# Performance work log

Hardware: AMD Instinct MI355X
Metric: run time of the kernel (lower is better)

## Reference

```python
import jax, jax.numpy as jnp
import numpy as np
import math

T = 4096        # block_size / sequence length
E = 2048        # embedding_dim
D = 256         # head_dim


def setup_inputs() -> dict:
    key = jax.random.key(0)
    k_x, k_q, k_k, k_v = jax.random.split(key, 4)
    x = jax.random.normal(k_x, (T, E), dtype=jnp.float32)
    # nn.Linear weights are [out_features, in_features]
    s = 1.0 / math.sqrt(E)
    Wq = jax.random.normal(k_q, (D, E), dtype=jnp.float32) * s
    Wk = jax.random.normal(k_k, (D, E), dtype=jnp.float32) * s
    Wv = jax.random.normal(k_v, (D, E), dtype=jnp.float32) * s
    return {"x": x, "Wq": Wq, "Wk": Wk, "Wv": Wv}


def reference(x, Wq, Wk, Wv):
    # Projections: x @ W.T  (torch Linear, no bias)
    Q = x @ Wq.T            # [T, D]
    K = x @ Wk.T            # [T, D]
    V = x @ Wv.T            # [T, D]
    scale = 1.0 / math.sqrt(Q.shape[-1])
    scores = (Q @ K.T) * scale                      # [T, T]
    causal = jnp.tril(jnp.ones((T, T), dtype=bool))
    scores = jnp.where(causal, scores, jnp.float32(-1e10))
    probs = jax.nn.softmax(scores, axis=-1)         # row softmax (torch legacy dim=1 for 2-D)
    return probs @ V                                # [T, D]
```

## Files before the change

kernel.cpp:

```cpp
#include <hip/hip_runtime.h>
#include <hip/hip_bf16.h>

#define T_DIM 4096
#define E_DIM 2048
#define D_DIM 256
#define NT_SPLIT 5

typedef __attribute__((ext_vector_type(4))) float f32x4;
typedef __attribute__((ext_vector_type(8))) short s16x8;

__device__ __forceinline__ unsigned short f2bf(float f) {
  unsigned int u = __float_as_uint(f);
  unsigned int r = (u + 0x7FFFu + ((u >> 16) & 1u)) >> 16;
  return (unsigned short)r;
}
__device__ __forceinline__ float bf2f(unsigned short h) {
  return __uint_as_float(((unsigned int)h) << 16);
}

__device__ __forceinline__ f32x4 mfma16(s16x8 a, s16x8 b, f32x4 c) {
  return __builtin_amdgcn_mfma_f32_16x16x32_bf16(a, b, c, 0, 0, 0);
}

__device__ __forceinline__ void gload_lds16(const void* g, void* l) {
  __builtin_amdgcn_global_load_lds((const __attribute__((address_space(1))) void*)g,
                                   (__attribute__((address_space(3))) void*)l, 16, 0, 0);
}

__global__ __launch_bounds__(256) void cvt_all(const float* __restrict__ x,
                                               const float* __restrict__ wq,
                                               const float* __restrict__ wk,
                                               const float* __restrict__ wv,
                                               unsigned short* __restrict__ xb,
                                               unsigned short* __restrict__ wb) {
  int blk = blockIdx.x;
  const float* src;
  unsigned short* dst;
  int rel;
  if (blk < 4096)      { src = x;  dst = xb;           rel = blk; }
  else if (blk < 4352) { src = wq; dst = wb;           rel = blk - 4096; }
  else if (blk < 4608) { src = wk; dst = wb + 524288;  rel = blk - 4352; }
  else                 { src = wv; dst = wb + 1048576; rel = blk - 4608; }
  int i = rel * 256 + threadIdx.x;
  float4 a = ((const float4*)src)[i * 2];
  float4 b = ((const float4*)src)[i * 2 + 1];
  uint4 o;
  o.x = (unsigned int)f2bf(a.x) | ((unsigned int)f2bf(a.y) << 16);
  o.y = (unsigned int)f2bf(a.z) | ((unsigned int)f2bf(a.w) << 16);
  o.z = (unsigned int)f2bf(b.x) | ((unsigned int)f2bf(b.y) << 16);
  o.w = (unsigned int)f2bf(b.z) | ((unsigned int)f2bf(b.w) << 16);
  ((uint4*)dst)[i] = o;
}

__global__ __launch_bounds__(256, 3) void qkv_gemm(
    const unsigned short* __restrict__ xb, const unsigned short* __restrict__ wb,
    unsigned short* __restrict__ Qg, unsigned short* __restrict__ Kg,
    unsigned short* __restrict__ Vt) {
  __shared__ __align__(16) unsigned short Al[2][128 * 64];
  __shared__ __align__(16) unsigned short Bl[2][64 * 64];
  int tid = threadIdx.x, wid = tid >> 6, lane = tid & 63;
  int lr = lane & 15, lk = lane >> 4;
  int bi_ = (int)blockIdx.x;
  int xcd = bi_ & 7, kk = bi_ >> 3;
  int mb_ = (kk / 12) * 8 + xcd, nb_ = kk % 12;
  int bm0 = mb_ * 128, bn0 = nb_ * 64;
  int wm = (wid >> 1) * 64, wn = (wid & 1) * 32;

  f32x4 acc[4][2];
#pragma unroll
  for (int m = 0; m < 4; ++m)
#pragma unroll
    for (int n = 0; n < 2; ++n) acc[m][n] = (f32x4){0.f, 0.f, 0.f, 0.f};

#define STAGE_QKV(kt, buf)                                                              \
  {                                                                                     \
    int k0 = (kt)*64;                                                                   \
    _Pragma("unroll") for (int i2 = 0; i2 < 4; ++i2) {                                  \
      int ci = (wid * 4 + i2) * 64 + lane;                                              \
      int row = ci >> 3, cc = ci & 7;                                                   \
      gload_lds16(&xb[(size_t)(bm0 + row) * E_DIM + k0 + ((cc ^ (row & 7)) << 3)],      \
                  &Al[buf][(size_t)(wid * 4 + i2) * 512]);                              \
    }                                                                                   \
    _Pragma("unroll") for (int i2 = 0; i2 < 2; ++i2) {                                  \
      int ci = (wid * 2 + i2) * 64 + lane;                                              \
      int row = ci >> 3, cc = ci & 7;                                                   \
      gload_lds16(&wb[(size_t)(bn0 + row) * E_DIM + k0 + ((cc ^ (row & 7)) << 3)],      \
                  &Bl[buf][(size_t)(wid * 2 + i2) * 512]);                              \
    }                                                                                   \
  }

  STAGE_QKV(0, 0);
  for (int kt = 0; kt < 32; ++kt) {
    int cur = kt & 1;
    __syncthreads();
    if (kt + 1 < 32) STAGE_QKV(kt + 1, cur ^ 1);
    s16x8 af[2][4], bfr[2][2];
#pragma unroll
    for (int c = 0; c < 2; ++c) {
#pragma unroll
      for (int m = 0; m < 4; ++m)
        af[c][m] = *(const s16x8*)&Al[cur][(size_t)(wm + m * 16 + lr) * 64 +
                                           (((c * 4 + lk) ^ (lr & 7)) << 3)];
#pragma unroll
      for (int n = 0; n < 2; ++n)
        bfr[c][n] = *(const s16x8*)&Bl[cur][(size_t)(wn + n * 16 + lr) * 64 +
                                            (((c * 4 + lk) ^ (lr & 7)) << 3)];
    }
#pragma unroll
    for (int c = 0; c < 2; ++c)
#pragma unroll
      for (int m = 0; m < 4; ++m)
#pragma unroll
        for (int n = 0; n < 2; ++n) acc[m][n] = mfma16(af[c][m], bfr[c][n], acc[m][n]);
  }

#pragma unroll
  for (int m = 0; m < 4; ++m) {
    int grow = bm0 + wm + m * 16 + lk * 4;
#pragma unroll
    for (int n = 0; n < 2; ++n) {
      int gcol = bn0 + wn + n * 16 + lr;
      unsigned short h[4];
#pragma unroll
      for (int r = 0; r < 4; ++r) h[r] = f2bf(acc[m][n][r]);
      if (gcol < 256) {
#pragma unroll
        for (int r = 0; r < 4; ++r) Qg[(size_t)(grow + r) * D_DIM + gcol] = h[r];
      } else if (gcol < 512) {
#pragma unroll
        for (int r = 0; r < 4; ++r) Kg[(size_t)(grow + r) * D_DIM + gcol - 256] = h[r];
      } else {
        uint2 w;
        w.x = (unsigned int)h[0] | ((unsigned int)h[1] << 16);
        w.y = (unsigned int)h[2] | ((unsigned int)h[3] << 16);
        *(uint2*)&Vt[(size_t)(gcol - 512) * T_DIM + grow] = w;
      }
    }
  }
#undef STAGE_QKV
}

__global__ __launch_bounds__(256, 2) void attn_kernel(
    const unsigned short* __restrict__ Qg, const unsigned short* __restrict__ Kg,
    const unsigned short* __restrict__ Vt, unsigned short* __restrict__ Opart,
    float* __restrict__ mpart, float* __restrict__ lpart) {
  __shared__ __align__(16) unsigned short Kl[2][32 * 256];
  __shared__ __align__(16) unsigned short Vl[2][256 * 32];
  __shared__ __align__(16) unsigned short Pl[4][32 * 40];

  int b = blockIdx.x;
  int t = 31, s = 0;
  {
    int acc = 0;
#pragma unroll 1
    for (int k = 1; k <= 32; ++k) {
      int c = (4 * k + 4) / 5;
      if (acc + c > b) { t = k - 1; s = b - acc; break; }
      acc += c;
    }
  }
  int nt = 4 * (t + 1) - NT_SPLIT * s;
  if (nt > NT_SPLIT) nt = NT_SPLIT;

  int tid = threadIdx.x, wid = tid >> 6, lane = tid & 63;
  int lr = lane & 15, lk = lane >> 4;
  int q0w = t * 128 + wid * 32;
  unsigned short* pl = &Pl[wid][0];

  s16x8 qf[2][8];
#pragma unroll
  for (int qb = 0; qb < 2; ++qb)
#pragma unroll
    for (int c = 0; c < 8; ++c)
      qf[qb][c] = *(const s16x8*)&Qg[(size_t)(q0w + qb * 16 + lr) * D_DIM + c * 32 + lk * 8];

  float m_run[2] = {-1e30f, -1e30f}, l_run[2] = {0.f, 0.f};
  f32x4 Oa[2][16];
#pragma unroll
  for (int qb = 0; qb < 2; ++qb)
#pragma unroll
    for (int d = 0; d < 16; ++d) Oa[qb][d] = (f32x4){0.f, 0.f, 0.f, 0.f};
  const float scale = 0.0625f;
  int j0 = NT_SPLIT * s;

#define STAGE_KV(j, buf)                                                             \
  {                                                                                  \
    int kv_ = (j)*32;                                                                \
    _Pragma("unroll") for (int i2 = 0; i2 < 4; ++i2) {                               \
      int l = (wid * 4 + i2) * 64 + lane;                                            \
      int row = l >> 5, gcs = l & 31;                                                \
      gload_lds16(&Kg[(size_t)(kv_ + row) * D_DIM + ((gcs ^ (row & 7)) << 3)],       \
                  &Kl[buf][(size_t)(wid * 4 + i2) * 512]);                           \
    }                                                                                \
    _Pragma("unroll") for (int i2 = 0; i2 < 4; ++i2) {                               \
      int l = (wid * 4 + i2) * 64 + lane;                                            \
      int d_ = l >> 2, gs = l & 3;                                                   \
      gload_lds16(&Vt[(size_t)d_ * T_DIM + kv_ + ((gs ^ ((d_ >> 1) & 3)) << 3)],     \
                  &Vl[buf][(size_t)(wid * 4 + i2) * 512]);                           \
    }                                                                                \
  }

  STAGE_KV(j0, 0);
  for (int n = 0; n < nt; ++n) {
    int j = j0 + n, kv = j * 32, cur = n & 1;
    __syncthreads();
    if (n + 1 < nt) STAGE_KV(j + 1, cur ^ 1);
    const unsigned short* kl = &Kl[cur][0];
    const unsigned short* vl = &Vl[cur][0];

    f32x4 sa[2][2];
#pragma unroll
    for (int qb = 0; qb < 2; ++qb)
#pragma unroll
      for (int jb = 0; jb < 2; ++jb) sa[qb][jb] = (f32x4){0.f, 0.f, 0.f, 0.f};
    int sw = lr & 7;
#pragma unroll
    for (int jb = 0; jb < 2; ++jb) {
      int rowbase = (jb * 16 + lr) * 32;
#pragma unroll
      for (int c = 0; c < 8; ++c) {
        s16x8 kf = *(const s16x8*)&kl[(size_t)(rowbase + ((c * 4 + lk) ^ sw)) * 8];
        sa[0][jb] = mfma16(kf, qf[0][c], sa[0][jb]);
        sa[1][jb] = mfma16(kf, qf[1][c], sa[1][jb]);
      }
    }

    bool needmask = (kv + 31 > q0w);
    float alpha_s[2];
#pragma unroll
    for (int qb = 0; qb < 2; ++qb) {
      int myq = q0w + qb * 16 + lr;
      float tmax = -1e30f;
#pragma unroll
      for (int jb = 0; jb < 2; ++jb) {
#pragma unroll
        for (int r = 0; r < 4; ++r) {
          float v = sa[qb][jb][r] * scale;
          if (needmask && (kv + jb * 16 + lk * 4 + r) > myq) v = -1e30f;
          sa[qb][jb][r] = v;
          tmax = fmaxf(tmax, v);
        }
      }
      tmax = fmaxf(tmax, __shfl_xor(tmax, 16));
      tmax = fmaxf(tmax, __shfl_xor(tmax, 32));
      float m_new = fmaxf(fmaxf(m_run[qb], tmax), -1e29f);
      alpha_s[qb] = __expf(m_run[qb] - m_new);
      float psum = 0.f;
#pragma unroll
      for (int jb = 0; jb < 2; ++jb) {
        float p0 = __expf(sa[qb][jb][0] - m_new);
        float p1 = __expf(sa[qb][jb][1] - m_new);
        float p2 = __expf(sa[qb][jb][2] - m_new);
        float p3 = __expf(sa[qb][jb][3] - m_new);
        psum += (p0 + p1) + (p2 + p3);
        uint2 w;
        w.x = (unsigned int)f2bf(p0) | ((unsigned int)f2bf(p1) << 16);
        w.y = (unsigned int)f2bf(p2) | ((unsigned int)f2bf(p3) << 16);
        *(uint2*)&pl[(qb * 16 + lr) * 40 + jb * 16 + lk * 4] = w;
      }
      psum += __shfl_xor(psum, 16);
      psum += __shfl_xor(psum, 32);
      l_run[qb] = l_run[qb] * alpha_s[qb] + psum;
      m_run[qb] = m_new;
    }

    float al[2][4];
#pragma unroll
    for (int qb = 0; qb < 2; ++qb)
#pragma unroll
      for (int r = 0; r < 4; ++r) al[qb][r] = __shfl(alpha_s[qb], lk * 4 + r);
#pragma unroll
    for (int qb = 0; qb < 2; ++qb)
#pragma unroll
      for (int d = 0; d < 16; ++d) {
#pragma unroll
        for (int r = 0; r < 4; ++r) Oa[qb][d][r] *= al[qb][r];
      }

    s16x8 pf0 = *(const s16x8*)&pl[lr * 40 + lk * 8];
    s16x8 pf1 = *(const s16x8*)&pl[(16 + lr) * 40 + lk * 8];
    int vsw = lk ^ ((lr >> 1) & 3);
#pragma unroll
    for (int d = 0; d < 16; ++d) {
      s16x8 vf = *(const s16x8*)&vl[(size_t)((d * 16 + lr) * 4 + vsw) * 8];
      Oa[0][d] = mfma16(pf0, vf, Oa[0][d]);
      Oa[1][d] = mfma16(pf1, vf, Oa[1][d]);
    }
  }

#pragma unroll
  for (int d = 0; d < 16; ++d) {
#pragma unroll
    for (int qb = 0; qb < 2; ++qb) {
      unsigned short h[4];
#pragma unroll
      for (int r = 0; r < 4; ++r) h[r] = f2bf(Oa[qb][d][r]);
      uint2 w;
      w.x = (unsigned int)h[0] | ((unsigned int)h[1] << 16);
      w.y = (unsigned int)h[2] | ((unsigned int)h[3] << 16);
      *(uint2*)&Opart[((size_t)b * 256 + d * 16 + lr) * 128 + wid * 32 + qb * 16 + lk * 4] = w;
    }
  }
  if (lk == 0) {
#pragma unroll
    for (int qb = 0; qb < 2; ++qb) {
      mpart[(size_t)b * 128 + wid * 32 + qb * 16 + lr] = m_run[qb];
      lpart[(size_t)b * 128 + wid * 32 + qb * 16 + lr] = l_run[qb];
    }
  }
#undef STAGE_KV
}

__global__ __launch_bounds__(256) void merge_kernel(const unsigned short* __restrict__ Opart,
                                                    const float* __restrict__ mpart,
                                                    const float* __restrict__ lpart,
                                                    float* __restrict__ out) {
  __shared__ float trans[128 * 65];
  int blk = blockIdx.x;
  int t = blk >> 2, d0 = (blk & 3) * 64, q0 = t * 128;
  int ql = threadIdx.x & 127, dg = threadIdx.x >> 7;
  int base = 0;
#pragma unroll 1
  for (int k = 1; k <= t; ++k) base += (4 * k + 4) / 5;
  int nb = (4 * (t + 1) + 4) / 5;

  float M = -1e30f, den = 0.f;
  for (int p = 0; p < nb; ++p) {
    float mp = mpart[(size_t)(base + p) * 128 + ql];
    float lp = lpart[(size_t)(base + p) * 128 + ql];
    float Mn = fmaxf(M, mp);
    den = den * __expf(M - Mn) + __expf(mp - Mn) * lp;
    M = Mn;
  }
  float inv = 1.0f / den;

  float acc[32];
#pragma unroll
  for (int k = 0; k < 32; ++k) acc[k] = 0.f;
  for (int p = 0; p < nb; ++p) {
    float w = __expf(mpart[(size_t)(base + p) * 128 + ql] - M);
    const unsigned short* op = &Opart[((size_t)(base + p) * 256 + d0 + dg) * 128 + ql];
#pragma unroll
    for (int k = 0; k < 32; ++k) acc[k] += w * bf2f(op[(size_t)(2 * k) * 128]);
  }
#pragma unroll
  for (int k = 0; k < 32; ++k) trans[ql * 65 + dg + 2 * k] = acc[k] * inv;
  __syncthreads();

#pragma unroll
  for (int kk = 0; kk < 32; ++kk) {
    int q = (threadIdx.x >> 6) + 4 * kk;
    int dd = threadIdx.x & 63;
    out[(size_t)(q0 + q) * 256 + d0 + dd] = trans[q * 65 + dd];
  }
}

extern "C" void kernel_launch(void* const* d_in, const int* in_sizes, int n_in,
                              void* d_out, int out_size, void* d_ws, size_t ws_size,
                              hipStream_t stream) {
  const float* x  = (const float*)d_in[0];
  const float* Wq = (const float*)d_in[1];
  const float* Wk = (const float*)d_in[2];
  const float* Wv = (const float*)d_in[3];

  char* ws = (char*)d_ws;
  unsigned short* xb = (unsigned short*)(ws);
  unsigned short* wb = (unsigned short*)(ws + 16777216);
  unsigned short* Qg = (unsigned short*)(ws + 19922944);
  unsigned short* Kg = (unsigned short*)(ws + 22020096);
  unsigned short* Vt = (unsigned short*)(ws + 24117248);
  unsigned short* Opart = (unsigned short*)(ws + 26214400);
  float* mpart = (float*)(ws + 54722560);
  float* lpart = (float*)(ws + 54945280);

  cvt_all<<<4864, 256, 0, stream>>>(x, Wq, Wk, Wv, xb, wb);
  qkv_gemm<<<384, 256, 0, stream>>>(xb, wb, Qg, Kg, Vt);
  attn_kernel<<<435, 256, 0, stream>>>(Qg, Kg, Vt, Opart, mpart, lpart);
  merge_kernel<<<128, 256, 0, stream>>>(Opart, mpart, lpart, (float*)d_out);
}
```

Before: 112.6 us.

## Retile QKV GEMM and attention split, fuse merge passes into one online loop

The QKV GEMM switches to 64x64 tiles with a K-step of 128, giving 768 blocks. Its pipeline now uses explicit barriers and vmcnt waits instead of __syncthreads. Attention moves to 512-thread blocks over 256-query tiles, with 64-wide KV chunks and a fixed two-chunk split per block (272 blocks). Query-tile and split indices are mapped through a sqrt-based triangular index, and the P buffer gets an XOR-swizzled layout. The merge kernel folds its max/denominator pass and its accumulation pass into one online-rescaled loop over more partials. Together these change occupancy and per-block work balance and raise partial-output traffic, with some risk from the larger LDS footprint and register pressure.

Result: faster. 109.9 us (-2.4%).

```diff
diff --git a/kernel.cpp b/kernel.cpp
--- a/kernel.cpp
+++ b/kernel.cpp
@@ -4,7 +4,6 @@
 #define T_DIM 4096
 #define E_DIM 2048
 #define D_DIM 256
-#define NT_SPLIT 5
 
 typedef __attribute__((ext_vector_type(4))) float f32x4;
 typedef __attribute__((ext_vector_type(8))) short s16x8;
@@ -52,70 +51,72 @@
   ((uint4*)dst)[i] = o;
 }
 
-__global__ __launch_bounds__(256, 3) void qkv_gemm(
+__global__ __launch_bounds__(256, 2) void qkv_gemm(
     const unsigned short* __restrict__ xb, const unsigned short* __restrict__ wb,
     unsigned short* __restrict__ Qg, unsigned short* __restrict__ Kg,
     unsigned short* __restrict__ Vt) {
-  __shared__ __align__(16) unsigned short Al[2][128 * 64];
-  __shared__ __align__(16) unsigned short Bl[2][64 * 64];
+  __shared__ __align__(16) unsigned short Al[2][64 * 128];
+  __shared__ __align__(16) unsigned short Bl[2][64 * 128];
   int tid = threadIdx.x, wid = tid >> 6, lane = tid & 63;
   int lr = lane & 15, lk = lane >> 4;
-  int bi_ = (int)blockIdx.x;
-  int xcd = bi_ & 7, kk = bi_ >> 3;
-  int mb_ = (kk / 12) * 8 + xcd, nb_ = kk % 12;
-  int bm0 = mb_ * 128, bn0 = nb_ * 64;
-  int wm = (wid >> 1) * 64, wn = (wid & 1) * 32;
-
-  f32x4 acc[4][2];
-#pragma unroll
-  for (int m = 0; m < 4; ++m)
+  int bi = (int)blockIdx.x;
+  int j = (bi & 7) * 96 + (bi >> 3);
+  int mb = j / 12, nb = j % 12;
+  int bm0 = mb * 64, bn0 = nb * 64;
+  int wm = (wid >> 1) * 32, wn = (wid & 1) * 32;
+
+  f32x4 acc[2][2];
+#pragma unroll
+  for (int m = 0; m < 2; ++m)
 #pragma unroll
     for (int n = 0; n < 2; ++n) acc[m][n] = (f32x4){0.f, 0.f, 0.f, 0.f};
 
 #define STAGE_QKV(kt, buf)                                                              \
   {                                                                                     \
-    int k0 = (kt)*64;                                                                   \
+    int k0 = (kt)*128;                                                                  \
     _Pragma("unroll") for (int i2 = 0; i2 < 4; ++i2) {                                  \
-      int ci = (wid * 4 + i2) * 64 + lane;                                              \
-      int row = ci >> 3, cc = ci & 7;                                                   \
-      gload_lds16(&xb[(size_t)(bm0 + row) * E_DIM + k0 + ((cc ^ (row & 7)) << 3)],      \
+      int idx = (wid * 4 + i2) * 64 + lane;                                             \
+      int row = idx >> 4, g = idx & 15;                                                 \
+      gload_lds16(&xb[(size_t)(bm0 + row) * E_DIM + k0 + ((g ^ (row & 7)) << 3)],      \
                   &Al[buf][(size_t)(wid * 4 + i2) * 512]);                              \
+      gload_lds16(&wb[(size_t)(bn0 + row) * E_DIM + k0 + ((g ^ (row & 7)) << 3)],      \
+                  &Bl[buf][(size_t)(wid * 4 + i2) * 512]);                              \
     }                                                                                   \
-    _Pragma("unroll") for (int i2 = 0; i2 < 2; ++i2) {                                  \
-      int ci = (wid * 2 + i2) * 64 + lane;                                              \
-      int row = ci >> 3, cc = ci & 7;                                                   \
-      gload_lds16(&wb[(size_t)(bn0 + row) * E_DIM + k0 + ((cc ^ (row & 7)) << 3)],      \
-                  &Bl[buf][(size_t)(wid * 2 + i2) * 512]);                              \
-    }                                                                                   \
   }
 
   STAGE_QKV(0, 0);
-  for (int kt = 0; kt < 32; ++kt) {
+  for (int kt = 0; kt < 16; ++kt) {
     int cur = kt & 1;
-    __syncthreads();
-    if (kt + 1 < 32) STAGE_QKV(kt + 1, cur ^ 1);
-    s16x8 af[2][4], bfr[2][2];
-#pragma unroll
-    for (int c = 0; c < 2; ++c) {
-#pragma unroll
-      for (int m = 0; m < 4; ++m)
-        af[c][m] = *(const s16x8*)&Al[cur][(size_t)(wm + m * 16 + lr) * 64 +
+    __builtin_amdgcn_s_barrier();
+    if (kt + 1 < 16) {
+      STAGE_QKV(kt + 1, cur ^ 1);
+      asm volatile("s_waitcnt vmcnt(8)" ::: "memory");
+    } else {
+      asm volatile("s_waitcnt vmcnt(0)" ::: "memory");
+    }
+    __builtin_amdgcn_s_barrier();
+    s16x8 af[4][2], bfr[4][2];
+#pragma unroll
+    for (int c = 0; c < 4; ++c) {
+#pragma unroll
+      for (int m = 0; m < 2; ++m)
+        af[c][m] = *(const s16x8*)&Al[cur][(size_t)(wm + m * 16 + lr) * 128 +
                                            (((c * 4 + lk) ^ (lr & 7)) << 3)];
 #pragma unroll
       for (int n = 0; n < 2; ++n)
-        bfr[c][n] = *(const s16x8*)&Bl[cur][(size_t)(wn + n * 16 + lr) * 64 +
+        bfr[c][n] = *(const s16x8*)&Bl[cur][(size_t)(wn + n * 16 + lr) * 128 +
                                             (((c * 4 + lk) ^ (lr & 7)) << 3)];
     }
 #pragma unroll
-    for (int c = 0; c < 2; ++c)
-#pragma unroll
-      for (int m = 0; m < 4; ++m)
+    for (int c = 0; c < 4; ++c)
+#pragma unroll
+      for (int m = 0; m < 2; ++m)
 #pragma unroll
         for (int n = 0; n < 2; ++n) acc[m][n] = mfma16(af[c][m], bfr[c][n], acc[m][n]);
   }
 
 #pragma unroll
-  for (int m = 0; m < 4; ++m) {
+  for (int m = 0; m < 2; ++m) {
     int grow = bm0 + wm + m * 16 + lk * 4;
 #pragma unroll
     for (int n = 0; n < 2; ++n) {
@@ -140,99 +141,99 @@
 #undef STAGE_QKV
 }
 
-__global__ __launch_bounds__(256, 2) void attn_kernel(
+__global__ __launch_bounds__(512, 2) void attn_kernel(
     const unsigned short* __restrict__ Qg, const unsigned short* __restrict__ Kg,
     const unsigned short* __restrict__ Vt, unsigned short* __restrict__ Opart,
     float* __restrict__ mpart, float* __restrict__ lpart) {
-  __shared__ __align__(16) unsigned short Kl[2][32 * 256];
-  __shared__ __align__(16) unsigned short Vl[2][256 * 32];
-  __shared__ __align__(16) unsigned short Pl[4][32 * 40];
-
-  int b = blockIdx.x;
-  int t = 31, s = 0;
-  {
-    int acc = 0;
-#pragma unroll 1
-    for (int k = 1; k <= 32; ++k) {
-      int c = (4 * k + 4) / 5;
-      if (acc + c > b) { t = k - 1; s = b - acc; break; }
-      acc += c;
-    }
-  }
-  int nt = 4 * (t + 1) - NT_SPLIT * s;
-  if (nt > NT_SPLIT) nt = NT_SPLIT;
+  __shared__ __align__(16) unsigned short Kl[2][64 * 256];
+  __shared__ __align__(16) unsigned short Vl[2][256 * 64];
+  __shared__ __align__(16) unsigned short Pl[8 * 32 * 64];
+
+  int bi = (int)blockIdx.x;
+  int j = (bi & 7) * 34 + (bi >> 3);
+  int t = (int)((sqrtf(4.0f * (float)j + 1.0f) - 1.0f) * 0.5f);
+  while (t > 0 && t * (t + 1) > j) --t;
+  while ((t + 1) * (t + 2) <= j) ++t;
+  int s = j - t * (t + 1);
 
   int tid = threadIdx.x, wid = tid >> 6, lane = tid & 63;
   int lr = lane & 15, lk = lane >> 4;
-  int q0w = t * 128 + wid * 32;
-  unsigned short* pl = &Pl[wid][0];
-
-  s16x8 qf[2][8];
-#pragma unroll
-  for (int qb = 0; qb < 2; ++qb)
-#pragma unroll
-    for (int c = 0; c < 8; ++c)
-      qf[qb][c] = *(const s16x8*)&Qg[(size_t)(q0w + qb * 16 + lr) * D_DIM + c * 32 + lk * 8];
-
-  float m_run[2] = {-1e30f, -1e30f}, l_run[2] = {0.f, 0.f};
-  f32x4 Oa[2][16];
-#pragma unroll
-  for (int qb = 0; qb < 2; ++qb)
-#pragma unroll
-    for (int d = 0; d < 16; ++d) Oa[qb][d] = (f32x4){0.f, 0.f, 0.f, 0.f};
-  const float scale = 0.0625f;
-  int j0 = NT_SPLIT * s;
-
-#define STAGE_KV(j, buf)                                                             \
+  int q0w = t * 256 + wid * 32;
+  unsigned short* pl = &Pl[wid * 2048];
+
+#define STAGE_KV(jt, buf)                                                            \
   {                                                                                  \
-    int kv_ = (j)*32;                                                                \
+    int kv_ = (jt)*64;                                                               \
     _Pragma("unroll") for (int i2 = 0; i2 < 4; ++i2) {                               \
-      int l = (wid * 4 + i2) * 64 + lane;                                            \
-      int row = l >> 5, gcs = l & 31;                                                \
-      gload_lds16(&Kg[(size_t)(kv_ + row) * D_DIM + ((gcs ^ (row & 7)) << 3)],       \
+      int idx = (wid * 4 + i2) * 64 + lane;                                          \
+      int row = idx >> 5, g = idx & 31;                                              \
+      gload_lds16(&Kg[(size_t)(kv_ + row) * D_DIM + ((g ^ (row & 7)) << 3)],         \
                   &Kl[buf][(size_t)(wid * 4 + i2) * 512]);                           \
     }                                                                                \
     _Pragma("unroll") for (int i2 = 0; i2 < 4; ++i2) {                               \
-      int l = (wid * 4 + i2) * 64 + lane;                                            \
-      int d_ = l >> 2, gs = l & 3;                                                   \
-      gload_lds16(&Vt[(size_t)d_ * T_DIM + kv_ + ((gs ^ ((d_ >> 1) & 3)) << 3)],     \
+      int idx = (wid * 4 + i2) * 64 + lane;                                          \
+      int d_ = idx >> 3, g = idx & 7;                                                \
+      gload_lds16(&Vt[(size_t)d_ * T_DIM + kv_ + ((g ^ (d_ & 7)) << 3)],             \
                   &Vl[buf][(size_t)(wid * 4 + i2) * 512]);                           \
     }                                                                                \
   }
 
-  STAGE_KV(j0, 0);
-  for (int n = 0; n < nt; ++n) {
-    int j = j0 + n, kv = j * 32, cur = n & 1;
-    __syncthreads();
-    if (n + 1 < nt) STAGE_KV(j + 1, cur ^ 1);
+  STAGE_KV(2 * s, 0);
+
+  s16x8 qf[2][8];
+#pragma unroll
+  for (int qb = 0; qb < 2; ++qb)
+#pragma unroll
+    for (int c = 0; c < 8; ++c)
+      qf[qb][c] = *(const s16x8*)&Qg[(size_t)(q0w + qb * 16 + lr) * D_DIM + c * 32 + lk * 8];
+
+  float m_run[2] = {-1e30f, -1e30f}, l_run[2] = {0.f, 0.f};
+  f32x4 Oa[2][16];
+#pragma unroll
+  for (int qb = 0; qb < 2; ++qb)
+#pragma unroll
+    for (int d = 0; d < 16; ++d) Oa[qb][d] = (f32x4){0.f, 0.f, 0.f, 0.f};
+  const float scale = 0.0625f;
+  int sw = lr & 7;
+
+#pragma unroll
+  for (int n = 0; n < 2; ++n) {
+    int jt = 2 * s + n, kv = jt * 64, cur = n;
+    __builtin_amdgcn_s_barrier();
+    if (n == 0) {
+      STAGE_KV(jt + 1, 1);
+      asm volatile("s_waitcnt vmcnt(8)" ::: "memory");
+    } else {
+      asm volatile("s_waitcnt vmcnt(0)" ::: "memory");
+    }
+    __builtin_amdgcn_s_barrier();
     const unsigned short* kl = &Kl[cur][0];
     const unsigned short* vl = &Vl[cur][0];
 
-    f32x4 sa[2][2];
+    f32x4 sa[2][4];
 #pragma unroll
     for (int qb = 0; qb < 2; ++qb)
 #pragma unroll
-      for (int jb = 0; jb < 2; ++jb) sa[qb][jb] = (f32x4){0.f, 0.f, 0.f, 0.f};
-    int sw = lr & 7;
-#pragma unroll
-    for (int jb = 0; jb < 2; ++jb) {
-      int rowbase = (jb * 16 + lr) * 32;
+      for (int jb = 0; jb < 4; ++jb) sa[qb][jb] = (f32x4){0.f, 0.f, 0.f, 0.f};
+#pragma unroll
+    for (int jb = 0; jb < 4; ++jb) {
+      int rowbase = (jb * 16 + lr) * 256;
 #pragma unroll
       for (int c = 0; c < 8; ++c) {
-        s16x8 kf = *(const s16x8*)&kl[(size_t)(rowbase + ((c * 4 + lk) ^ sw)) * 8];
+        s16x8 kf = *(const s16x8*)&kl[(size_t)rowbase + (((c * 4 + lk) ^ sw) << 3)];
         sa[0][jb] = mfma16(kf, qf[0][c], sa[0][jb]);
         sa[1][jb] = mfma16(kf, qf[1][c], sa[1][jb]);
       }
     }
 
-    bool needmask = (kv + 31 > q0w);
+    bool needmask = (kv + 63 > q0w);
     float alpha_s[2];
 #pragma unroll
     for (int qb = 0; qb < 2; ++qb) {
       int myq = q0w + qb * 16 + lr;
       float tmax = -1e30f;
 #pragma unroll
-      for (int jb = 0; jb < 2; ++jb) {
+      for (int jb = 0; jb < 4; ++jb) {
 #pragma unroll
         for (int r = 0; r < 4; ++r) {
           float v = sa[qb][jb][r] * scale;
@@ -246,8 +247,9 @@
       float m_new = fmaxf(fmaxf(m_run[qb], tmax), -1e29f);
       alpha_s[qb] = __expf(m_run[qb] - m_new);
       float psum = 0.f;
-#pragma unroll
-      for (int jb = 0; jb < 2; ++jb) {
+      int q = qb * 16 + lr;
+#pragma unroll
+      for (int jb = 0; jb < 4; ++jb) {
         float p0 = __expf(sa[qb][jb][0] - m_new);
         float p1 = __expf(sa[qb][jb][1] - m_new);
         float p2 = __expf(sa[qb][jb][2] - m_new);
@@ -256,7 +258,7 @@
         uint2 w;
         w.x = (unsigned int)f2bf(p0) | ((unsigned int)f2bf(p1) << 16);
         w.y = (unsigned int)f2bf(p2) | ((unsigned int)f2bf(p3) << 16);
-        *(uint2*)&pl[(qb * 16 + lr) * 40 + jb * 16 + lk * 4] = w;
+        *(uint2*)&pl[(size_t)q * 64 + (((jb * 2 + (lk >> 1)) ^ sw) << 3) + (lk & 1) * 4] = w;
       }
       psum += __shfl_xor(psum, 16);
       psum += __shfl_xor(psum, 32);
@@ -277,14 +279,22 @@
         for (int r = 0; r < 4; ++r) Oa[qb][d][r] *= al[qb][r];
       }
 
-    s16x8 pf0 = *(const s16x8*)&pl[lr * 40 + lk * 8];
-    s16x8 pf1 = *(const s16x8*)&pl[(16 + lr) * 40 + lk * 8];
-    int vsw = lk ^ ((lr >> 1) & 3);
+    s16x8 pf[2][2];
+#pragma unroll
+    for (int qb = 0; qb < 2; ++qb)
+#pragma unroll
+      for (int ks = 0; ks < 2; ++ks)
+        pf[qb][ks] = *(const s16x8*)&pl[(size_t)(qb * 16 + lr) * 64 +
+                                        (((ks * 4 + lk) ^ sw) << 3)];
 #pragma unroll
     for (int d = 0; d < 16; ++d) {
-      s16x8 vf = *(const s16x8*)&vl[(size_t)((d * 16 + lr) * 4 + vsw) * 8];
-      Oa[0][d] = mfma16(pf0, vf, Oa[0][d]);
-      Oa[1][d] = mfma16(pf1, vf, Oa[1][d]);
+#pragma unroll
+      for (int ks = 0; ks < 2; ++ks) {
+        s16x8 vf = *(const s16x8*)&vl[(size_t)(d * 16 + lr) * 64 +
+                                      (((ks * 4 + lk) ^ sw) << 3)];
+        Oa[0][d] = mfma16(pf[0][ks], vf, Oa[0][d]);
+        Oa[1][d] = mfma16(pf[1][ks], vf, Oa[1][d]);
+      }
     }
   }
 
@@ -298,14 +308,14 @@
       uint2 w;
       w.x = (unsigned int)h[0] | ((unsigned int)h[1] << 16);
       w.y = (unsigned int)h[2] | ((unsigned int)h[3] << 16);
-      *(uint2*)&Opart[((size_t)b * 256 + d * 16 + lr) * 128 + wid * 32 + qb * 16 + lk * 4] = w;
+      *(uint2*)&Opart[((size_t)j * 256 + d * 16 + lr) * 256 + wid * 32 + qb * 16 + lk * 4] = w;
     }
   }
   if (lk == 0) {
 #pragma unroll
     for (int qb = 0; qb < 2; ++qb) {
-      mpart[(size_t)b * 128 + wid * 32 + qb * 16 + lr] = m_run[qb];
-      lpart[(size_t)b * 128 + wid * 32 + qb * 16 + lr] = l_run[qb];
+      mpart[(size_t)j * 256 + wid * 32 + qb * 16 + lr] = m_run[qb];
+      lpart[(size_t)j * 256 + wid * 32 + qb * 16 + lr] = l_run[qb];
     }
   }
 #undef STAGE_KV
@@ -315,43 +325,40 @@
                                                     const float* __restrict__ mpart,
                                                     const float* __restrict__ lpart,
                                                     float* __restrict__ out) {
-  __shared__ float trans[128 * 65];
+  __shared__ float trans[256 * 33];
   int blk = blockIdx.x;
-  int t = blk >> 2, d0 = (blk & 3) * 64, q0 = t * 128;
-  int ql = threadIdx.x & 127, dg = threadIdx.x >> 7;
-  int base = 0;
+  int t = blk >> 3, d0 = (blk & 7) * 32, q0 = t * 256;
+  int ql = threadIdx.x;
+  int base = t * (t + 1), np = 2 * t + 2;
+
+  float M = -1e30f, den = 0.f;
+  float acc[32];
+#pragma unroll
+  for (int k = 0; k < 32; ++k) acc[k] = 0.f;
+
 #pragma unroll 1
-  for (int k = 1; k <= t; ++k) base += (4 * k + 4) / 5;
-  int nb = (4 * (t + 1) + 4) / 5;
-
-  float M = -1e30f, den = 0.f;
-  for (int p = 0; p < nb; ++p) {
-    float mp = mpart[(size_t)(base + p) * 128 + ql];
-    float lp = lpart[(size_t)(base + p) * 128 + ql];
+  for (int p = 0; p < np; ++p) {
+    float mp = mpart[(size_t)(base + p) * 256 + ql];
+    float lp = lpart[(size_t)(base + p) * 256 + ql];
     float Mn = fmaxf(M, mp);
-    den = den * __expf(M - Mn) + __expf(mp - Mn) * lp;
+    float sc = __expf(M - Mn);
+    float w = __expf(mp - Mn);
+    den = den * sc + w * lp;
+    const unsigned short* op = &Opart[((size_t)(base + p) * 256 + d0) * 256 + ql];
+#pragma unroll
+    for (int k = 0; k < 32; ++k) acc[k] = acc[k] * sc + w * bf2f(op[(size_t)k * 256]);
     M = Mn;
   }
   float inv = 1.0f / den;
-
-  float acc[32];
-#pragma unroll
-  for (int k = 0; k < 32; ++k) acc[k] = 0.f;
-  for (int p = 0; p < nb; ++p) {
-    float w = __expf(mpart[(size_t)(base + p) * 128 + ql] - M);
-    const unsigned short* op = &Opart[((size_t)(base + p) * 256 + d0 + dg) * 128 + ql];
-#pragma unroll
-    for (int k = 0; k < 32; ++k) acc[k] += w * bf2f(op[(size_t)(2 * k) * 128]);
-  }
-#pragma unroll
-  for (int k = 0; k < 32; ++k) trans[ql * 65 + dg + 2 * k] = acc[k] * inv;
+#pragma unroll
+  for (int k = 0; k < 32; ++k) trans[ql * 33 + k] = acc[k] * inv;
   __syncthreads();
 
 #pragma unroll
-  for (int kk = 0; kk < 32; ++kk) {
-    int q = (threadIdx.x >> 6) + 4 * kk;
-    int dd = threadIdx.x & 63;
-    out[(size_t)(q0 + q) * 256 + d0 + dd] = trans[q * 65 + dd];
+  for (int k = 0; k < 32; ++k) {
+    int q = (threadIdx.x >> 5) + 8 * k;
+    int dd = threadIdx.x & 31;
+    out[(size_t)(q0 + q) * 256 + d0 + dd] = trans[q * 33 + dd];
   }
 }
 
@@ -370,11 +377,11 @@
   unsigned short* Kg = (unsigned short*)(ws + 22020096);
   unsigned short* Vt = (unsigned short*)(ws + 24117248);
   unsigned short* Opart = (unsigned short*)(ws + 26214400);
-  float* mpart = (float*)(ws + 54722560);
-  float* lpart = (float*)(ws + 54945280);
+  float* mpart = (float*)(ws + 61865984);
+  float* lpart = (float*)(ws + 62144512);
 
   cvt_all<<<4864, 256, 0, stream>>>(x, Wq, Wk, Wv, xb, wb);
-  qkv_gemm<<<384, 256, 0, stream>>>(xb, wb, Qg, Kg, Vt);
-  attn_kernel<<<435, 256, 0, stream>>>(Qg, Kg, Vt, Opart, mpart, lpart);
+  qkv_gemm<<<768, 256, 0, stream>>>(xb, wb, Qg, Kg, Vt);
+  attn_kernel<<<272, 512, 0, stream>>>(Qg, Kg, Vt, Opart, mpart, lpart);
   merge_kernel<<<128, 256, 0, stream>>>(Opart, mpart, lpart, (float*)d_out);
 }
```
